# Optimization experiments

Hardware: AMD Instinct MI355X
Metric: run time of the kernel (lower is better)

Reference implementation:

```python
import jax, jax.numpy as jnp
import numpy as np

D_MODEL = 1024
NUM_HEADS = 16
HEAD_DIM = D_MODEL // NUM_HEADS  # used only for score scaling, as in the torch code


def setup_inputs() -> dict:
    key = jax.random.key(0)
    ks = jax.random.split(key, 8)
    B, S, D = 4, 2048, D_MODEL
    w_scale = 1.0 / np.sqrt(D)
    return {
        "x": jax.random.normal(ks[0], (B, S, D), dtype=jnp.float32),
        "Wq": jax.random.normal(ks[1], (D, D), dtype=jnp.float32) * w_scale,
        "bq": jnp.zeros((D,), dtype=jnp.float32),
        "Wk": jax.random.normal(ks[2], (D, D), dtype=jnp.float32) * w_scale,
        "bk": jnp.zeros((D,), dtype=jnp.float32),
        "Wv": jax.random.normal(ks[3], (D, D), dtype=jnp.float32) * w_scale,
        "bv": jnp.zeros((D,), dtype=jnp.float32),
        "temperature_scale": jnp.ones((1,), dtype=jnp.float32),
    }


def reference(x, Wq, bq, Wk, bk, Wv, bv, temperature_scale):
    # q, k, v: (B, S, D) -- no head split in the original module
    q = x @ Wq + bq
    k = x @ Wk + bk
    v = x @ Wv + bv
    scale = jnp.asarray(HEAD_DIM, x.dtype) ** 0.5
    # scores: (B, S, S)
    scores = jnp.einsum("bqd,bkd->bqk", q, k) / scale / temperature_scale[0]
    probs = jax.nn.softmax(scores, axis=-1)
    # per-row attention entropy (B, S, 1)
    entropy = -jnp.sum(probs * jnp.log(probs + 1e-8), axis=-1, keepdims=True)
    attention_output = jnp.einsum("bqk,bkd->bqd", probs, v)
    return attention_output, entropy.mean()
```

## Files before the change

### kernel.cpp

```cpp
#include <hip/hip_runtime.h>
#include <hip/hip_bf16.h>
#include <cstdint>
#include <cstddef>


typedef __attribute__((ext_vector_type(8))) short short8;
typedef __attribute__((ext_vector_type(4))) short short4v;
typedef __attribute__((ext_vector_type(4))) float f32x4;

#define GLOBAL_AS __attribute__((address_space(1)))
#define LDS_AS __attribute__((address_space(3)))

__device__ __forceinline__ void async_load16(const void* g, void* lds) {
  __builtin_amdgcn_global_load_lds((GLOBAL_AS void*)g, (LDS_AS void*)lds, 16, 0, 0);
}

__device__ __forceinline__ short f2bf_s(float x) {
  __hip_bfloat16 h = __float2bfloat16(x);
  return *reinterpret_cast<short*>(&h);
}

template <int MODE>
__device__ __forceinline__
void gemm256_body(const __hip_bfloat16* __restrict__ A,
                  const __hip_bfloat16* __restrict__ Bt,
                  void* __restrict__ Cout,
                  const float* __restrict__ bias,
                  int K, int lda, int ldb, int ldc,
                  __hip_bfloat16* __restrict__ sA,
                  __hip_bfloat16* __restrict__ sB,
                  int m0, int n0,
                  const float* __restrict__ aux,
                  float* __restrict__ stats) {
  const int tid  = threadIdx.x;
  const int lane = tid & 63;
  const int wid  = tid >> 6;
  const int wm   = (wid >> 2) * 128;
  const int wn   = (wid & 3) * 64;
  const int quad = lane >> 4;
  const int rc   = lane & 15;
  const int rc7  = rc & 7;
  const int wnr  = wn & 64;

  f32x4 acc[8][4] = {};

  const int r0   = tid >> 3;
  const int scol = ((tid & 7) ^ (r0 & 7)) * 8;
  const __hip_bfloat16* Ag = A  + (size_t)(m0 + r0) * lda + scol;
  const __hip_bfloat16* Bg = Bt + (size_t)(n0 + r0) * ldb + scol;

  const int NT = K >> 6;

  auto stA = [&](int buf, int half, int kofs) {
    const __hip_bfloat16* s = Ag + (size_t)(half * 128) * lda + kofs;
    __hip_bfloat16* d = sA + (size_t)buf * 16384 + (size_t)half * 8192 + tid * 8;
    async_load16(s, d);
    async_load16(s + (size_t)64 * lda, d + 4096);
  };
  auto stB = [&](int buf, int half, int kofs) {
    const __hip_bfloat16* s = Bg + (size_t)(half * 128) * ldb + kofs;
    __hip_bfloat16* d = sB + (size_t)buf * 16384 + (size_t)half * 8192 + tid * 8;
    async_load16(s, d);
    async_load16(s + (size_t)64 * ldb, d + 4096);
  };

  const __hip_bfloat16* sAh = sA + (size_t)(wm >> 7) * 8192;
  const __hip_bfloat16* sBh = sB + (size_t)(wn >> 7) * 8192;

  short8 af[2][4], ah[2][4], blo[2][2], bhi[2][2];

  {
    const int k1 = (NT > 1) ? 64 : 0;
    stA(0, 0, 0);  stA(0, 1, 0);  stB(0, 0, 0);  stB(0, 1, 0);
    stA(1, 0, k1); stA(1, 1, k1); stB(1, 0, k1); stB(1, 1, k1);
  }
  asm volatile("s_waitcnt vmcnt(8)" ::: "memory");
  __builtin_amdgcn_s_barrier();
#pragma unroll
  for (int kk = 0; kk < 2; ++kk) {
    const int gs = ((kk * 4 + quad) ^ rc7) * 8;
#pragma unroll
    for (int i = 0; i < 4; ++i)
      af[kk][i] = *(const short8*)&sAh[(i * 16 + rc) * 64 + gs];
#pragma unroll
    for (int j = 0; j < 2; ++j)
      blo[kk][j] = *(const short8*)&sBh[(wnr + j * 16 + rc) * 64 + gs];
  }

  for (int t = 0; t < NT; ++t) {
    const int buf = t & 1;
    const __hip_bfloat16* sAc = sAh + buf * 16384;
    const __hip_bfloat16* sBc = sBh + buf * 16384;
    const __hip_bfloat16* sAn = sAh + (buf ^ 1) * 16384;
    const __hip_bfloat16* sBn = sBh + (buf ^ 1) * 16384;
    const int k2 = ((t + 2 < NT) ? t + 2 : NT - 1) * 64;

#pragma unroll
    for (int kk = 0; kk < 2; ++kk) {
      const int gs = ((kk * 4 + quad) ^ rc7) * 8;
#pragma unroll
      for (int i = 0; i < 4; ++i)
        ah[kk][i] = *(const short8*)&sAc[((i + 4) * 16 + rc) * 64 + gs];
    }
    __builtin_amdgcn_s_barrier();
    __builtin_amdgcn_s_setprio(1);
#pragma unroll
    for (int mi = 0; mi < 4; ++mi)
#pragma unroll
      for (int ni = 0; ni < 2; ++ni)
#pragma unroll
        for (int kk = 0; kk < 2; ++kk)
          acc[mi][ni] = __builtin_amdgcn_mfma_f32_16x16x32_bf16(
              af[kk][mi], blo[kk][ni], acc[mi][ni], 0, 0, 0);
    __builtin_amdgcn_s_setprio(0);
    __builtin_amdgcn_s_barrier();

    stA(buf, 0, k2);
#pragma unroll
    for (int kk = 0; kk < 2; ++kk) {
      const int gs = ((kk * 4 + quad) ^ rc7) * 8;
#pragma unroll
      for (int j = 0; j < 2; ++j)
        bhi[kk][j] = *(const short8*)&sBc[(wnr + (j + 2) * 16 + rc) * 64 + gs];
    }
    __builtin_amdgcn_s_barrier();
    __builtin_amdgcn_s_setprio(1);
#pragma unroll
    for (int mi = 0; mi < 4; ++mi)
#pragma unroll
      for (int ni = 0; ni < 2; ++ni)
#pragma unroll
        for (int kk = 0; kk < 2; ++kk)
          acc[4 + mi][ni] = __builtin_amdgcn_mfma_f32_16x16x32_bf16(
              ah[kk][mi], blo[kk][ni], acc[4 + mi][ni], 0, 0, 0);
    __builtin_amdgcn_s_setprio(0);
    __builtin_amdgcn_s_barrier();

    asm volatile("s_waitcnt vmcnt(2)" ::: "memory");
    stA(buf, 1, k2);
    stB(buf, 0, k2);
#pragma unroll
    for (int kk = 0; kk < 2; ++kk) {
      const int gs = ((kk * 4 + quad) ^ rc7) * 8;
#pragma unroll
      for (int j = 0; j < 2; ++j)
        blo[kk][j] = *(const short8*)&sBn[(wnr + j * 16 + rc) * 64 + gs];
    }
    __builtin_amdgcn_s_barrier();
    __builtin_amdgcn_s_setprio(1);
#pragma unroll
    for (int mi = 0; mi < 4; ++mi)
#pragma unroll
      for (int nj = 0; nj < 2; ++nj)
#pragma unroll
        for (int kk = 0; kk < 2; ++kk)
          acc[mi][2 + nj] = __builtin_amdgcn_mfma_f32_16x16x32_bf16(
              af[kk][mi], bhi[kk][nj], acc[mi][2 + nj], 0, 0, 0);
    __builtin_amdgcn_s_setprio(0);
    __builtin_amdgcn_s_barrier();

    stB(buf, 1, k2);
#pragma unroll
    for (int kk = 0; kk < 2; ++kk) {
      const int gs = ((kk * 4 + quad) ^ rc7) * 8;
#pragma unroll
      for (int i = 0; i < 4; ++i)
        af[kk][i] = *(const short8*)&sAn[(i * 16 + rc) * 64 + gs];
    }
    __builtin_amdgcn_s_barrier();
    __builtin_amdgcn_s_setprio(1);
#pragma unroll
    for (int mi = 0; mi < 4; ++mi)
#pragma unroll
      for (int nj = 0; nj < 2; ++nj)
#pragma unroll
        for (int kk = 0; kk < 2; ++kk)
          acc[4 + mi][2 + nj] = __builtin_amdgcn_mfma_f32_16x16x32_bf16(
              ah[kk][mi], bhi[kk][nj], acc[4 + mi][2 + nj], 0, 0, 0);
    __builtin_amdgcn_s_setprio(0);
    __builtin_amdgcn_s_barrier();
  }
  asm volatile("s_waitcnt vmcnt(0)" ::: "memory");

  if (MODE == 3) {
    const int chunk = (n0 + wn) >> 6;
#pragma unroll
    for (int mi = 0; mi < 8; ++mi) {
      float l_acc[4] = {}, w_acc[4] = {};
#pragma unroll
      for (int ni = 0; ni < 4; ++ni)
#pragma unroll
        for (int r = 0; r < 4; ++r) {
          const float xv = acc[mi][ni][r];
          const float e = __expf(xv);
          acc[mi][ni][r] = e;
          l_acc[r] += e;
          w_acc[r] += e * xv;
        }
#pragma unroll
      for (int r = 0; r < 4; ++r) {
        float l = l_acc[r], w = w_acc[r];
#pragma unroll
        for (int off = 1; off < 16; off <<= 1) {
          l += __shfl_xor(l, off);
          w += __shfl_xor(w, off);
        }
        if (rc == 0) {
          const int row = m0 + wm + mi * 16 + quad * 4 + r;
          *(float2*)&stats[((size_t)row * 32 + chunk) * 2] = make_float2(l, w);
        }
      }
#pragma unroll
      for (int ni = 0; ni < 4; ++ni) {
        const int col = n0 + wn + ni * 16 + rc;
#pragma unroll
        for (int r = 0; r < 4; ++r) {
          const int row = m0 + wm + mi * 16 + quad * 4 + r;
          ((__hip_bfloat16*)Cout)[(size_t)row * ldc + col] =
              __float2bfloat16(acc[mi][ni][r]);
        }
      }
    }
  } else {
    const float qsc = (MODE == 1 && aux) ? 1.0f / (8.0f * aux[0]) : 1.0f;
#pragma unroll
    for (int mi = 0; mi < 8; ++mi) {
#pragma unroll
      for (int ni = 0; ni < 4; ++ni) {
        const int col = n0 + wn + ni * 16 + rc;
        const float badd = bias[col];
        if (MODE == 2) {
          const int rowb = m0 + wm + mi * 16 + quad * 4;
          short4v o;
#pragma unroll
          for (int r = 0; r < 4; ++r) o[r] = f2bf_s(acc[mi][ni][r] + badd);
          const size_t idx = (size_t)(rowb >> 11) * (1024u * 2048u) +
                             (size_t)col * 2048u + (size_t)(rowb & 2047);
          *(short4v*)((short*)Cout + idx) = o;
        } else {
#pragma unroll
          for (int r = 0; r < 4; ++r) {
            const int row = m0 + wm + mi * 16 + quad * 4 + r;
            ((__hip_bfloat16*)Cout)[(size_t)row * ldc + col] =
                __float2bfloat16((acc[mi][ni][r] + badd) * qsc);
          }
        }
      }
    }
  }
}

__global__ __launch_bounds__(512, 2)
void qkv_fused256(const __hip_bfloat16* __restrict__ xb,
                  const __hip_bfloat16* __restrict__ Wt,
                  __hip_bfloat16* __restrict__ qb, __hip_bfloat16* __restrict__ kb,
                  __hip_bfloat16* __restrict__ vt,
                  const float* __restrict__ bq, const float* __restrict__ bk,
                  const float* __restrict__ bv, const float* __restrict__ tptr) {
  extern __shared__ __align__(16) __hip_bfloat16 smem[];
  __hip_bfloat16* sA = smem;
  __hip_bfloat16* sB = smem + 32768;
  const int lin = blockIdx.x;
  const int G  = (lin & 7) * 48 + (lin >> 3);
  const int mt = G / 12, nt = G % 12;
  const int m0  = mt * 256;
  const int n0g = nt * 256;
  const int z   = n0g >> 10;
  const int n0  = n0g & 1023;
  const __hip_bfloat16* B = Wt + (size_t)z * 1024 * 1024;
  if (z == 0)
    gemm256_body<1>(xb, B, qb, bq, 1024, 1024, 1024, 1024, sA, sB, m0, n0, tptr, nullptr);
  else if (z == 1)
    gemm256_body<1>(xb, B, kb, bk, 1024, 1024, 1024, 1024, sA, sB, m0, n0, nullptr, nullptr);
  else
    gemm256_body<2>(xb, B, vt, bv, 1024, 1024, 1024, 0, sA, sB, m0, n0, nullptr, nullptr);
}

__global__ __launch_bounds__(512, 2)
void scores256(const __hip_bfloat16* __restrict__ qb,
               const __hip_bfloat16* __restrict__ kb,
               __hip_bfloat16* __restrict__ Pt,
               float* __restrict__ stats) {
  extern __shared__ __align__(16) __hip_bfloat16 smem[];
  __hip_bfloat16* sA = smem;
  __hip_bfloat16* sB = smem + 32768;
  const int lin = blockIdx.x;
  const int G = (lin & 7) * 32 + (lin >> 3);
  const int z = G >> 6;
  const int r = G & 63;
  const int y = r >> 3, x = r & 7;
  gemm256_body<3>(qb + (size_t)z * 2048 * 1024, kb + (size_t)z * 2048 * 1024,
                  Pt + (size_t)z * 2048 * 2048, nullptr, 1024, 1024, 1024, 2048,
                  sA, sB, y * 256, x * 256, nullptr, stats + (size_t)z * 2048 * 64);
}

template <int MODE>
__device__ __forceinline__
void gemm_body(const __hip_bfloat16* __restrict__ A,
               const __hip_bfloat16* __restrict__ Bt,
               void* __restrict__ Cout,
               const float* __restrict__ bias,
               int K, int lda, int ldb, int ldc,
               __hip_bfloat16* __restrict__ sA,
               __hip_bfloat16* __restrict__ sB,
               int m0, int n0,
               const float* __restrict__ aux,
               float* __restrict__ stats) {
  const int tid  = threadIdx.x;
  const int lane = tid & 63;
  const int wid  = tid >> 6;
  const int wm = (wid >> 1) * 64;
  const int wn = (wid & 1) * 64;
  const int quad = lane >> 4;
  const int rc   = lane & 15;

  f32x4 acc[4][4] = {};

  const int srow = tid >> 3;
  const int scol = ((tid & 7) ^ ((tid >> 3) & 7)) * 8;
  const __hip_bfloat16* Ag = A  + (size_t)(m0 + srow) * lda + scol;
  const __hip_bfloat16* Bg = Bt + (size_t)(n0 + srow) * ldb + scol;

  for (int k0 = 0; k0 < K; k0 += 64) {
#pragma unroll
    for (int p = 0; p < 4; ++p) {
      async_load16(Ag + k0 + (size_t)(32 * p) * lda, &sA[(wid * 64 + 256 * p) * 8]);
      async_load16(Bg + k0 + (size_t)(32 * p) * ldb, &sB[(wid * 64 + 256 * p) * 8]);
    }
    __syncthreads();

#pragma unroll
    for (int kk = 0; kk < 2; ++kk) {
      const int xo = ((kk * 4 + quad) ^ (rc & 7)) * 8;
      short8 af[4], bf[4];
#pragma unroll
      for (int i = 0; i < 4; ++i)
        af[i] = *(const short8*)&sA[(wm + i * 16 + rc) * 64 + xo];
#pragma unroll
      for (int i = 0; i < 4; ++i)
        bf[i] = *(const short8*)&sB[(wn + i * 16 + rc) * 64 + xo];

#pragma unroll
      for (int mi = 0; mi < 4; ++mi)
#pragma unroll
        for (int ni = 0; ni < 4; ++ni)
          acc[mi][ni] = __builtin_amdgcn_mfma_f32_16x16x32_bf16(
              af[mi], bf[ni], acc[mi][ni], 0, 0, 0);
    }
    __syncthreads();
  }

  if (MODE == 4) {
#pragma unroll
    for (int mi = 0; mi < 4; ++mi) {
      float sc[4];
#pragma unroll
      for (int r = 0; r < 4; ++r)
        sc[r] = aux[m0 + wm + mi * 16 + quad * 4 + r];
#pragma unroll
      for (int ni = 0; ni < 4; ++ni) {
        const int col = n0 + wn + ni * 16 + rc;
#pragma unroll
        for (int r = 0; r < 4; ++r) {
          const int row = m0 + wm + mi * 16 + quad * 4 + r;
          ((float*)Cout)[(size_t)row * ldc + col] = acc[mi][ni][r] * sc[r];
        }
      }
    }
  }
}

__global__ __launch_bounds__(256)
void pv_swz(const __hip_bfloat16* __restrict__ Pt,
            const __hip_bfloat16* __restrict__ vt,
            float* __restrict__ out,
            const float* __restrict__ inv_l) {
  __shared__ __align__(16) __hip_bfloat16 sA[128 * 64];
  __shared__ __align__(16) __hip_bfloat16 sB[128 * 64];
  const int lin = blockIdx.x;
  const int j = lin & 7, t = lin >> 3;
  const int w = t & 3;
  const int G = j + 8 * (t >> 2);
  const size_t z = G >> 5;
  const int r = G & 31;
  const int y = (r >> 2) * 2 + (w >> 1);
  const int x = (r & 3) * 2 + (w & 1);
  gemm_body<4>(Pt + z * 2048 * 2048, vt + z * 1024 * 2048,
               out + z * 2048 * 1024, nullptr, 2048, 2048, 2048, 1024,
               sA, sB, y * 128, x * 128, inv_l + z * 2048, nullptr);
}

__global__ __launch_bounds__(256)
void cast_f32_to_bf16(const float* __restrict__ src,
                      __hip_bfloat16* __restrict__ dst, int n) {
  const int i = (blockIdx.x * 256 + threadIdx.x) * 8;
  if (i >= n) return;
  const float4 a = *(const float4*)(src + i);
  const float4 b = *(const float4*)(src + i + 4);
  short8 o;
  o[0] = f2bf_s(a.x); o[1] = f2bf_s(a.y); o[2] = f2bf_s(a.z); o[3] = f2bf_s(a.w);
  o[4] = f2bf_s(b.x); o[5] = f2bf_s(b.y); o[6] = f2bf_s(b.z); o[7] = f2bf_s(b.w);
  *(short8*)((short*)dst + i) = o;
}

__global__ __launch_bounds__(256)
void transpose_cast_3w(const float* __restrict__ Wq, const float* __restrict__ Wk,
                       const float* __restrict__ Wv,
                       __hip_bfloat16* __restrict__ Wt) {
  __shared__ float tile[64][65];
  const int z = blockIdx.z;
  const float* src = (z == 0) ? Wq : (z == 1) ? Wk : Wv;
  __hip_bfloat16* dst = Wt + (size_t)z * 1024 * 1024;
  const int c0 = blockIdx.x * 64;
  const int r0 = blockIdx.y * 64;
  const int lane = threadIdx.x & 63;
  const int grp  = threadIdx.x >> 6;
#pragma unroll
  for (int i = 0; i < 16; ++i) {
    const int r = grp * 16 + i;
    tile[r][lane] = src[(size_t)(r0 + r) * 1024 + c0 + lane];
  }
  __syncthreads();
#pragma unroll
  for (int i = 0; i < 16; ++i) {
    const int r = grp * 16 + i;
    dst[(size_t)(c0 + r) * 1024 + r0 + lane] = __float2bfloat16(tile[lane][r]);
  }
}

__global__ __launch_bounds__(256)
void stats_reduce(const float* __restrict__ stats,
                  float* __restrict__ inv_l, float* __restrict__ Hrow) {
  const int row = blockIdx.x * 256 + threadIdx.x;
  const float* sp = stats + (size_t)row * 64;
  float l = 0.f, w = 0.f;
#pragma unroll
  for (int j = 0; j < 16; ++j) {
    const float4 a = *(const float4*)(sp + j * 4);
    l += a.x + a.z;
    w += a.y + a.w;
  }
  const float il = 1.0f / l;
  inv_l[row] = il;
  Hrow[row] = __logf(l) - w * il;
}

__global__ __launch_bounds__(256)
void reduce_entropy(const float* __restrict__ Hrow, float* __restrict__ out) {
  const int tid  = threadIdx.x;
  const int lane = tid & 63;
  const int wid  = tid >> 6;
  float s = 0.f;
#pragma unroll
  for (int j = 0; j < 8; ++j) {
    const float4 a = *(const float4*)(Hrow + j * 1024 + tid * 4);
    s += a.x + a.y + a.z + a.w;
  }
#pragma unroll
  for (int off = 1; off < 64; off <<= 1) s += __shfl_xor(s, off);
  __shared__ float red[4];
  if (lane == 0) red[wid] = s;
  __syncthreads();
  if (tid == 0)
    out[0] = (red[0] + red[1] + red[2] + red[3]) * (1.0f / 8192.0f);
}

extern "C" void kernel_launch(void* const* d_in, const int* in_sizes, int n_in,
                              void* d_out, int out_size, void* d_ws, size_t ws_size,
                              hipStream_t stream) {
  const float* x    = (const float*)d_in[0];
  const float* Wq   = (const float*)d_in[1];
  const float* bq   = (const float*)d_in[2];
  const float* Wk   = (const float*)d_in[3];
  const float* bk   = (const float*)d_in[4];
  const float* Wv   = (const float*)d_in[5];
  const float* bv   = (const float*)d_in[6];
  const float* temp = (const float*)d_in[7];
  float* out = (float*)d_out;
  char* ws = (char*)d_ws;

  __hip_bfloat16* qb    = (__hip_bfloat16*)(ws + 0);
  __hip_bfloat16* kb    = (__hip_bfloat16*)(ws + 16777216);
  __hip_bfloat16* vt    = (__hip_bfloat16*)(ws + 33554432);
  __hip_bfloat16* xb    = (__hip_bfloat16*)(ws + 50331648);
  __hip_bfloat16* Wt    = (__hip_bfloat16*)(ws + 67108864);
  __hip_bfloat16* Pt    = (__hip_bfloat16*)(ws + 73400320);
  float*          stats = (float*)(ws + 106954752);
  float*          inv_l = (float*)(ws + 109051904);
  float*          Hrow  = (float*)(ws + 109084672);

  static bool attr_done = false;
  if (!attr_done) {
    hipFuncSetAttribute((const void*)qkv_fused256,
                        hipFuncAttributeMaxDynamicSharedMemorySize, 131072);
    hipFuncSetAttribute((const void*)scores256,
                        hipFuncAttributeMaxDynamicSharedMemorySize, 131072);
    attr_done = true;
  }

  cast_f32_to_bf16<<<4096, 256, 0, stream>>>(x, xb, 8388608);
  transpose_cast_3w<<<dim3(16, 16, 3), 256, 0, stream>>>(Wq, Wk, Wv, Wt);

  qkv_fused256<<<384, 512, 131072, stream>>>(xb, Wt, qb, kb, vt, bq, bk, bv, temp);

  scores256<<<256, 512, 131072, stream>>>(qb, kb, Pt, stats);
  stats_reduce<<<32, 256, 0, stream>>>(stats, inv_l, Hrow);
  pv_swz<<<512, 256, 0, stream>>>(Pt, vt, out, inv_l);

  reduce_entropy<<<1, 256, 0, stream>>>(Hrow, out + 8388608);
}
```

Measured before the change: 263.6 us.

## Merge prep kernels and restructure 256-tile GEMM barriers and load schedule

Combines the x cast and the weight transpose-cast into one launch, removing a kernel launch and its tail. In the 256-tile GEMM, every s_barrier is wrapped in sched_barrier fences so the compiler cannot move instructions across phase boundaries. The stA(buf,0) prefetch is moved later, next to stB(buf,1), and the partial vmcnt(2) wait becomes a full vmcnt(0) wait. The stricter wait and the tighter scheduling fences may expose more global-load latency in exchange for more predictable interleaving.

```diff
diff --git a/kernel.cpp b/kernel.cpp
--- a/kernel.cpp
+++ b/kernel.cpp
@@ -10,6 +10,13 @@
 
 #define GLOBAL_AS __attribute__((address_space(1)))
 #define LDS_AS __attribute__((address_space(3)))
+
+#define PHASE_BARRIER()                                   \
+  do {                                                    \
+    __builtin_amdgcn_sched_barrier(0);                    \
+    asm volatile("s_barrier" ::: "memory");               \
+    __builtin_amdgcn_sched_barrier(0);                    \
+  } while (0)
 
 __device__ __forceinline__ void async_load16(const void* g, void* lds) {
   __builtin_amdgcn_global_load_lds((GLOBAL_AS void*)g, (LDS_AS void*)lds, 16, 0, 0);
@@ -75,7 +82,7 @@
     stA(1, 0, k1); stA(1, 1, k1); stB(1, 0, k1); stB(1, 1, k1);
   }
   asm volatile("s_waitcnt vmcnt(8)" ::: "memory");
-  __builtin_amdgcn_s_barrier();
+  PHASE_BARRIER();
 #pragma unroll
   for (int kk = 0; kk < 2; ++kk) {
     const int gs = ((kk * 4 + quad) ^ rc7) * 8;
@@ -102,7 +109,7 @@
       for (int i = 0; i < 4; ++i)
         ah[kk][i] = *(const short8*)&sAc[((i + 4) * 16 + rc) * 64 + gs];
     }
-    __builtin_amdgcn_s_barrier();
+    PHASE_BARRIER();
     __builtin_amdgcn_s_setprio(1);
 #pragma unroll
     for (int mi = 0; mi < 4; ++mi)
@@ -113,9 +120,8 @@
           acc[mi][ni] = __builtin_amdgcn_mfma_f32_16x16x32_bf16(
               af[kk][mi], blo[kk][ni], acc[mi][ni], 0, 0, 0);
     __builtin_amdgcn_s_setprio(0);
-    __builtin_amdgcn_s_barrier();
-
-    stA(buf, 0, k2);
+    PHASE_BARRIER();
+
 #pragma unroll
     for (int kk = 0; kk < 2; ++kk) {
       const int gs = ((kk * 4 + quad) ^ rc7) * 8;
@@ -123,7 +129,7 @@
       for (int j = 0; j < 2; ++j)
         bhi[kk][j] = *(const short8*)&sBc[(wnr + (j + 2) * 16 + rc) * 64 + gs];
     }
-    __builtin_amdgcn_s_barrier();
+    PHASE_BARRIER();
     __builtin_amdgcn_s_setprio(1);
 #pragma unroll
     for (int mi = 0; mi < 4; ++mi)
@@ -134,9 +140,9 @@
           acc[4 + mi][ni] = __builtin_amdgcn_mfma_f32_16x16x32_bf16(
               ah[kk][mi], blo[kk][ni], acc[4 + mi][ni], 0, 0, 0);
     __builtin_amdgcn_s_setprio(0);
-    __builtin_amdgcn_s_barrier();
-
-    asm volatile("s_waitcnt vmcnt(2)" ::: "memory");
+    asm volatile("s_waitcnt vmcnt(0)" ::: "memory");
+    PHASE_BARRIER();
+
     stA(buf, 1, k2);
     stB(buf, 0, k2);
 #pragma unroll
@@ -146,7 +152,7 @@
       for (int j = 0; j < 2; ++j)
         blo[kk][j] = *(const short8*)&sBn[(wnr + j * 16 + rc) * 64 + gs];
     }
-    __builtin_amdgcn_s_barrier();
+    PHASE_BARRIER();
     __builtin_amdgcn_s_setprio(1);
 #pragma unroll
     for (int mi = 0; mi < 4; ++mi)
@@ -157,8 +163,9 @@
           acc[mi][2 + nj] = __builtin_amdgcn_mfma_f32_16x16x32_bf16(
               af[kk][mi], bhi[kk][nj], acc[mi][2 + nj], 0, 0, 0);
     __builtin_amdgcn_s_setprio(0);
-    __builtin_amdgcn_s_barrier();
-
+    PHASE_BARRIER();
+
+    stA(buf, 0, k2);
     stB(buf, 1, k2);
 #pragma unroll
     for (int kk = 0; kk < 2; ++kk) {
@@ -167,7 +174,7 @@
       for (int i = 0; i < 4; ++i)
         af[kk][i] = *(const short8*)&sAn[(i * 16 + rc) * 64 + gs];
     }
-    __builtin_amdgcn_s_barrier();
+    PHASE_BARRIER();
     __builtin_amdgcn_s_setprio(1);
 #pragma unroll
     for (int mi = 0; mi < 4; ++mi)
@@ -178,7 +185,7 @@
           acc[4 + mi][2 + nj] = __builtin_amdgcn_mfma_f32_16x16x32_bf16(
               ah[kk][mi], bhi[kk][nj], acc[4 + mi][2 + nj], 0, 0, 0);
     __builtin_amdgcn_s_setprio(0);
-    __builtin_amdgcn_s_barrier();
+    PHASE_BARRIER();
   }
   asm volatile("s_waitcnt vmcnt(0)" ::: "memory");
 
@@ -391,40 +398,39 @@
 }
 
 __global__ __launch_bounds__(256)
-void cast_f32_to_bf16(const float* __restrict__ src,
-                      __hip_bfloat16* __restrict__ dst, int n) {
-  const int i = (blockIdx.x * 256 + threadIdx.x) * 8;
-  if (i >= n) return;
-  const float4 a = *(const float4*)(src + i);
-  const float4 b = *(const float4*)(src + i + 4);
-  short8 o;
-  o[0] = f2bf_s(a.x); o[1] = f2bf_s(a.y); o[2] = f2bf_s(a.z); o[3] = f2bf_s(a.w);
-  o[4] = f2bf_s(b.x); o[5] = f2bf_s(b.y); o[6] = f2bf_s(b.z); o[7] = f2bf_s(b.w);
-  *(short8*)((short*)dst + i) = o;
-}
-
-__global__ __launch_bounds__(256)
-void transpose_cast_3w(const float* __restrict__ Wq, const float* __restrict__ Wk,
-                       const float* __restrict__ Wv,
-                       __hip_bfloat16* __restrict__ Wt) {
-  __shared__ float tile[64][65];
-  const int z = blockIdx.z;
-  const float* src = (z == 0) ? Wq : (z == 1) ? Wk : Wv;
-  __hip_bfloat16* dst = Wt + (size_t)z * 1024 * 1024;
-  const int c0 = blockIdx.x * 64;
-  const int r0 = blockIdx.y * 64;
-  const int lane = threadIdx.x & 63;
-  const int grp  = threadIdx.x >> 6;
-#pragma unroll
-  for (int i = 0; i < 16; ++i) {
-    const int r = grp * 16 + i;
-    tile[r][lane] = src[(size_t)(r0 + r) * 1024 + c0 + lane];
-  }
-  __syncthreads();
-#pragma unroll
-  for (int i = 0; i < 16; ++i) {
-    const int r = grp * 16 + i;
-    dst[(size_t)(c0 + r) * 1024 + r0 + lane] = __float2bfloat16(tile[lane][r]);
+void prep_fused(const float* __restrict__ x, __hip_bfloat16* __restrict__ xb,
+                const float* __restrict__ Wq, const float* __restrict__ Wk,
+                const float* __restrict__ Wv, __hip_bfloat16* __restrict__ Wt) {
+  if (blockIdx.x < 4096) {
+    const int i = (blockIdx.x * 256 + threadIdx.x) * 8;
+    const float4 a = *(const float4*)(x + i);
+    const float4 b = *(const float4*)(x + i + 4);
+    short8 o;
+    o[0] = f2bf_s(a.x); o[1] = f2bf_s(a.y); o[2] = f2bf_s(a.z); o[3] = f2bf_s(a.w);
+    o[4] = f2bf_s(b.x); o[5] = f2bf_s(b.y); o[6] = f2bf_s(b.z); o[7] = f2bf_s(b.w);
+    *(short8*)((short*)xb + i) = o;
+  } else {
+    __shared__ float tile[64][65];
+    const int b = blockIdx.x - 4096;
+    const int z = b >> 8;
+    const int rem = b & 255;
+    const int c0 = (rem & 15) * 64;
+    const int r0 = (rem >> 4) * 64;
+    const float* src = (z == 0) ? Wq : (z == 1) ? Wk : Wv;
+    __hip_bfloat16* dst = Wt + (size_t)z * 1024 * 1024;
+    const int lane = threadIdx.x & 63;
+    const int grp  = threadIdx.x >> 6;
+#pragma unroll
+    for (int i = 0; i < 16; ++i) {
+      const int r = grp * 16 + i;
+      tile[r][lane] = src[(size_t)(r0 + r) * 1024 + c0 + lane];
+    }
+    __syncthreads();
+#pragma unroll
+    for (int i = 0; i < 16; ++i) {
+      const int r = grp * 16 + i;
+      dst[(size_t)(c0 + r) * 1024 + r0 + lane] = __float2bfloat16(tile[lane][r]);
+    }
   }
 }
 
@@ -498,8 +504,7 @@
     attr_done = true;
   }
 
-  cast_f32_to_bf16<<<4096, 256, 0, stream>>>(x, xb, 8388608);
-  transpose_cast_3w<<<dim3(16, 16, 3), 256, 0, stream>>>(Wq, Wk, Wv, Wt);
+  prep_fused<<<4864, 256, 0, stream>>>(x, xb, Wq, Wk, Wv, Wt);
 
   qkv_fused256<<<384, 512, 131072, stream>>>(xb, Wt, qb, kb, vt, bq, bk, bv, temp);
 
```

Result: no change. 261.7 us (-0.7%).
